# Kernel optimization log

Measured on AMD Instinct MI355X. Metric: run time of the kernel, lower is better.

The kernel has to match this reference:

```python
import jax, jax.numpy as jnp
import numpy as np

K_MODES, L_LAYERS, N_CH, FEAT = 4, 8, 12, 64
BN_EPS = 1e-5


def setup_inputs() -> dict:
    key = jax.random.key(0)
    ks = jax.random.split(key, 12)
    B, T, C, NC = 64, 4096, N_CH, 10
    x = jax.random.normal(ks[0], (B, T, C), jnp.float32)
    # UVMD learnable params (torch init values)
    alpha = jnp.full((L_LAYERS, K_MODES), 100.0, jnp.float32)
    tau = jnp.full((L_LAYERS,), 0.05, jnp.float32)
    omega = jnp.linspace(0.05, 0.45, K_MODES, dtype=jnp.float32)
    def w(k, shape, fan_in):
        return jax.random.normal(k, shape, jnp.float32) * (1.0 / np.sqrt(fan_in))
    # K stacked per-band conv encoders: (K, O, I, kw)
    W1 = w(ks[1], (K_MODES, 32, C, 7), C * 7)
    W2 = w(ks[2], (K_MODES, 64, 32, 5), 32 * 5)
    W3 = w(ks[3], (K_MODES, FEAT, 64, 3), 64 * 3)
    b1 = jnp.zeros((K_MODES, 32)); g1 = jnp.ones((K_MODES, 32)); be1 = jnp.zeros((K_MODES, 32))
    b2 = jnp.zeros((K_MODES, 64)); g2 = jnp.ones((K_MODES, 64)); be2 = jnp.zeros((K_MODES, 64))
    b3 = jnp.zeros((K_MODES, FEAT)); g3 = jnp.ones((K_MODES, FEAT)); be3 = jnp.zeros((K_MODES, FEAT))
    enc_dim = K_MODES * FEAT
    Wc1 = w(ks[4], (128, enc_dim), enc_dim); bc1 = jnp.zeros((128,))
    Wc2 = w(ks[5], (NC, 128), 128); bc2 = jnp.zeros((NC,))
    return dict(x=x, alpha=alpha, tau=tau, omega=omega,
                W1=W1, b1=b1, g1=g1, be1=be1,
                W2=W2, b2=b2, g2=g2, be2=be2,
                W3=W3, b3=b3, g3=g3, be3=be3,
                Wc1=Wc1, bc1=bc1, Wc2=Wc2, bc2=bc2)


def _conv1d(x, w, b):
    # x: (B, Cin, T), w: (O, I, kw), 'same' padding
    pad = (w.shape[-1] - 1) // 2
    y = jax.lax.conv_general_dilated(x, w, (1,), [(pad, pad)],
                                     dimension_numbers=('NCH', 'OIH', 'NCH'))
    return y + b[None, :, None]


def _bn_eval(x, g, b):
    # BatchNorm1d eval with running_mean=0, running_var=1
    return x * (g / jnp.sqrt(1.0 + BN_EPS))[None, :, None] + b[None, :, None]


def _uvmd(x, alpha, tau, omega):
    B, T, C = x.shape
    x_flat = jnp.transpose(x, (0, 2, 1)).reshape(B * C, T)
    X = jnp.fft.rfft(x_flat, n=T)                         # (B*C, T//2+1) complex
    freqs = jnp.linspace(0.0, 0.5, T // 2 + 1).astype(jnp.float32)
    lam = jnp.zeros_like(X)
    u = [jnp.zeros_like(X) for _ in range(K_MODES)]
    total = jnp.zeros_like(X)                             # running sum of u_hats (Gauss-Seidel)
    for l in range(L_LAYERS):
        for k in range(K_MODES):
            residual = X - (total - u[k]) + lam / 2.0
            denom = 1.0 + alpha[l, k] * (freqs - omega[k]) ** 2
            new_u = residual / denom
            total = total - u[k] + new_u
            u[k] = new_u
        lam = lam + tau[l] * (X - total)
    modes = jnp.stack([jnp.fft.irfft(uk, n=T) for uk in u], axis=0)  # (K, B*C, T)
    return modes.reshape(K_MODES, B, C, T).transpose(1, 0, 3, 2)     # (B, K, T, C)


def reference(x, alpha, tau, omega,
              W1, b1, g1, be1, W2, b2, g2, be2, W3, b3, g3, be3,
              Wc1, bc1, Wc2, bc2):
    modes = _uvmd(x, alpha, tau, omega)           # (B, K, T, C)
    xk = jnp.transpose(modes, (1, 0, 3, 2))        # (K, B, C, T)

    def enc_one(xb, w1, bb1, gg1, bbe1, w2, bb2, gg2, bbe2, w3, bb3, gg3, bbe3):
        h = jax.nn.relu(_bn_eval(_conv1d(xb, w1, bb1), gg1, bbe1))
        h = jax.nn.relu(_bn_eval(_conv1d(h, w2, bb2), gg2, bbe2))
        h = jax.nn.relu(_bn_eval(_conv1d(h, w3, bb3), gg3, bbe3))
        return h.mean(axis=-1)                     # AdaptiveAvgPool1d(1)+Flatten -> (B, FEAT)

    feats = jax.vmap(enc_one)(xk, W1, b1, g1, be1, W2, b2, g2, be2, W3, b3, g3, be3)  # (K, B, FEAT)
    features = jnp.transpose(feats, (1, 0, 2)).reshape(feats.shape[1], -1)            # cat over k
    h = jax.nn.relu(features @ Wc1.T + bc1)        # Dropout is identity in eval
    logits = h @ Wc2.T + bc2
    return logits
```

## Files before the change

kernel.cpp:

```cpp
#include <hip/hip_runtime.h>
#include <math.h>

#define T_LEN 4096
#define NBINS 2049
#define B_SZ 64
#define C_IN 12
#define KM 4
#define FEAT 64

typedef __attribute__((ext_vector_type(8))) short short8v;
typedef __attribute__((ext_vector_type(4))) float floatx4;

__device__ __forceinline__ unsigned short f2bf(float f)
{
    unsigned int u = __float_as_uint(f);
    u += 0x7FFFu + ((u >> 16) & 1u);
    return (unsigned short)(u >> 16);
}

__device__ __forceinline__ int fphys(int i) { return i ^ ((i >> 4) & 15); }

__global__ void prep_all(const float* __restrict__ alpha,
                         const float* __restrict__ tau,
                         const float* __restrict__ omega,
                         const float* __restrict__ W1,
                         const float* __restrict__ W2,
                         const float* __restrict__ W3,
                         float2* __restrict__ tw4,
                         float* __restrict__ g,
                         float* __restrict__ feats,
                         unsigned short* __restrict__ Wp1,
                         unsigned short* __restrict__ Wp2,
                         unsigned short* __restrict__ Wp3)
{
    int gid = blockIdx.x * 256 + threadIdx.x;
    if (gid < 4096) {
        float ang = -(float)M_PI * (float)gid / 2048.0f;
        float sn, cs;
        sincosf(ang, &sn, &cs);
        tw4[gid] = make_float2(cs, sn);
        return;
    }
    gid -= 4096;
    if (gid < NBINS) {
        int f = gid;
        float freq = 0.5f * (float)f / 2048.0f;
        float a[4] = {0.f, 0.f, 0.f, 0.f};
        float s = 0.f, lamc = 0.f;
        for (int l = 0; l < 8; ++l) {
            for (int k = 0; k < 4; ++k) {
                float r = 1.f - (s - a[k]) + 0.5f * lamc;
                float d = freq - omega[k];
                float denom = 1.f + alpha[l * 4 + k] * d * d;
                float anew = r / denom;
                s += anew - a[k];
                a[k] = anew;
            }
            lamc += tau[l] * (1.f - s);
        }
        for (int k = 0; k < 4; ++k) g[k * NBINS + f] = a[k];
        return;
    }
    gid -= NBINS;
    if (gid < B_SZ * KM * FEAT) { feats[gid] = 0.f; return; }
    gid -= B_SZ * KM * FEAT;
    if (gid < KM * 4 * 32 * 32) {
        int i = gid;
        int kidx  = i & 31;
        int o     = (i >> 5) & 31;
        int dpair = (i >> 10) & 3;
        int k     = i >> 12;
        int d = dpair * 2 + (kidx >> 4);
        int c = kidx & 15;
        float v = (d < 7 && c < 12) ? W1[(((size_t)k * 32 + o) * 12 + c) * 7 + d] : 0.f;
        Wp1[(size_t)k * 4096 + dpair * 1024 + o * 32 + kidx] = f2bf(v);
        return;
    }
    gid -= KM * 4 * 32 * 32;
    if (gid < KM * 5 * 64 * 32) {
        int i = gid;
        int c = i & 31;
        int o = (i >> 5) & 63;
        int kd = i >> 11;
        int d = kd % 5, k = kd / 5;
        float v = W2[(((size_t)k * 64 + o) * 32 + c) * 5 + d];
        int sr = o >> 1;
        int q = (o & 1) * 4 + (c >> 3);
        int qp = q ^ (sr & 7);
        Wp2[(size_t)(k * 5 + d) * 2048 + sr * 64 + qp * 8 + (c & 7)] = f2bf(v);
        return;
    }
    gid -= KM * 5 * 64 * 32;
    if (gid < KM * 3 * 64 * 64) {
        int i = gid;
        int c = i & 63;
        int o = (i >> 6) & 63;
        int kd = i >> 12;
        int d = kd % 3, k = kd / 3;
        float v = W3[(((size_t)k * 64 + o) * 64 + c) * 3 + d];
        int blk = (c >> 3) ^ (o & 7);
        Wp3[(size_t)k * (3 * 64 * 64) + (d * 64 + o) * 64 + blk * 8 + (c & 7)] = f2bf(v);
        return;
    }
}

__device__ inline float2* fft_stages4(float2* bufA, float2* bufB,
                                      const float2* __restrict__ tw4, float syf)
{
    float2* src = bufA;
    float2* dst = bufB;
#pragma unroll
    for (int st = 0; st < 6; ++st) {
        const int sh = 2 * st;
        const int s = 1 << sh;
        for (int v = threadIdx.x; v < 1024; v += 512) {
            const int q = v & (s - 1);
            const int p = v >> sh;
            float2 a = src[fphys(v)];
            float2 b = src[fphys(v + 1024)];
            float2 c = src[fphys(v + 2048)];
            float2 d = src[fphys(v + 3072)];
            const int i1 = p << sh;
            float2 w1 = tw4[i1];
            float2 w2 = tw4[2 * i1];
            float2 w3 = tw4[3 * i1];
            float apcx = a.x + c.x, apcy = a.y + c.y;
            float amcx = a.x - c.x, amcy = a.y - c.y;
            float bpdx = b.x + d.x, bpdy = b.y + d.y;
            float sjx = -syf * (b.y - d.y);
            float sjy =  syf * (b.x - d.x);
            float2 x0 = make_float2(apcx + bpdx, apcy + bpdy);
            float t1x = amcx - sjx, t1y = amcy - sjy;
            float t2x = apcx - bpdx, t2y = apcy - bpdy;
            float t3x = amcx + sjx, t3y = amcy + sjy;
            float cs1 = w1.x, sn1 = syf * w1.y;
            float cs2 = w2.x, sn2 = syf * w2.y;
            float cs3 = w3.x, sn3 = syf * w3.y;
            float2 x1 = make_float2(cs1 * t1x - sn1 * t1y, cs1 * t1y + sn1 * t1x);
            float2 x2 = make_float2(cs2 * t2x - sn2 * t2y, cs2 * t2y + sn2 * t2x);
            float2 x3 = make_float2(cs3 * t3x - sn3 * t3y, cs3 * t3y + sn3 * t3x);
            const int ob = q + (p << (sh + 2));
            dst[fphys(ob)]         = x0;
            dst[fphys(ob + s)]     = x1;
            dst[fphys(ob + 2 * s)] = x2;
            dst[fphys(ob + 3 * s)] = x3;
        }
        __syncthreads();
        float2* tmp = src; src = dst; dst = tmp;
    }
    return src;
}

__global__ __launch_bounds__(512) void fft_fwd_packed(const float* __restrict__ x,
                                                      const float2* __restrict__ tw4,
                                                      float2* __restrict__ Xs)
{
    int rp = blockIdx.x;
    int b = rp / 6, c0 = (rp % 6) * 2;
    __shared__ float2 bufA[T_LEN];
    __shared__ float2 bufB[T_LEN];
    for (int t = threadIdx.x; t < T_LEN; t += 512) {
        const float* px = x + ((size_t)b * T_LEN + t) * C_IN + c0;
        bufA[fphys(t)] = make_float2(px[0], px[1]);
    }
    __syncthreads();
    float2* Z = fft_stages4(bufA, bufB, tw4, 1.f);
    size_t row = (size_t)b * C_IN + c0;
    for (int f = threadIdx.x; f <= 2048; f += 512) {
        float2 z  = Z[fphys(f)];
        float2 zm = Z[fphys((T_LEN - f) & (T_LEN - 1))];
        Xs[row * NBINS + f]       = make_float2(0.5f * (z.x + zm.x), 0.5f * (z.y - zm.y));
        Xs[(row + 1) * NBINS + f] = make_float2(0.5f * (z.y + zm.y), 0.5f * (zm.x - z.x));
    }
}

__global__ __launch_bounds__(512) void fft_inv_packed(const float2* __restrict__ Xs,
                                                      const float* __restrict__ g,
                                                      const float2* __restrict__ tw4,
                                                      unsigned int* __restrict__ modeU)
{
    int rp = blockIdx.x;
    int kk = blockIdx.y;
    int b = rp / 6, pr = rp % 6;
    int c0 = pr * 2;
    size_t rowa = (size_t)b * C_IN + c0;
    __shared__ float2 bufA[T_LEN];
    __shared__ float2 bufB[T_LEN];
    const float* gk = g + kk * NBINS;
    for (int f = threadIdx.x; f < T_LEN; f += 512) {
        int fe = (f <= 2048) ? f : (T_LEN - f);
        float2 A  = Xs[rowa * NBINS + fe];
        float2 Bv = Xs[(rowa + 1) * NBINS + fe];
        float gv = gk[fe];
        if (f > 2048) { A.y = -A.y; Bv.y = -Bv.y; }
        bufA[fphys(f)] = make_float2(gv * (A.x - Bv.y), gv * (A.y + Bv.x));
    }
    __syncthreads();
    float2* z = fft_stages4(bufA, bufB, tw4, -1.f);
    const float invn = 1.f / (float)T_LEN;
    unsigned int* plane = modeU + (((size_t)kk * B_SZ + b) * 6 + pr) * T_LEN;
    for (int t = threadIdx.x; t < T_LEN; t += 512) {
        float2 zz = z[fphys(t)];
        unsigned int pk = (unsigned int)f2bf(zz.x * invn) |
                          ((unsigned int)f2bf(zz.y * invn) << 16);
        plane[t] = pk;
    }
}

__global__ __launch_bounds__(256) void conv1_mfma(
    const unsigned int* __restrict__ modeU,
    const unsigned short* __restrict__ Wp1all,
    const float* __restrict__ bias,
    const float* __restrict__ gamma,
    const float* __restrict__ beta,
    unsigned short* __restrict__ h1bf)
{
    __shared__ __align__(16) char smem[4352 + 8192];
    char* Xl  = smem;
    char* rep = smem + 4352;

    const int b = blockIdx.y;
    const int kk = blockIdx.z;
    const int t0 = blockIdx.x * 128;
    const int tid = threadIdx.x;
    const unsigned int* planes = modeU + ((size_t)kk * B_SZ + b) * 6 * T_LEN;
    const unsigned short* Wp1 = Wp1all + (size_t)kk * 4096;
    const float* bi = bias + kk * 32;
    const float* ga = gamma + kk * 32;
    const float* be = beta + kk * 32;
    const int sr0 = t0 >> 2;

    for (int i = tid; i < 272; i += 256) {
        int p = i / 34;
        int tc = i % 34;
        int t_base = t0 - 4 + tc * 4;
        unsigned int vv[4] = {0u, 0u, 0u, 0u};
        if (p < 6) {
            const unsigned int* pl = planes + (size_t)p * T_LEN;
            if (t_base >= 0 && t_base + 3 < T_LEN) {
                uint4 v4 = *(const uint4*)(pl + t_base);
                vv[0] = v4.x; vv[1] = v4.y; vv[2] = v4.z; vv[3] = v4.w;
            } else {
#pragma unroll
                for (int e = 0; e < 4; ++e) {
                    int t = t_base + e;
                    vv[e] = (t >= 0 && t < T_LEN) ? pl[t] : 0u;
                }
            }
        }
        int cb = p >> 2, j = p & 3;
        int sr_g = t_base >> 2;
        int ls = sr_g - sr0 + 1;
        int key = sr_g & 7;
#pragma unroll
        for (int e = 0; e < 4; ++e) {
            int q = e * 2 + cb;
            int qp = q ^ key;
            *(unsigned int*)(Xl + (size_t)ls * 128 + qp * 16 + j * 4) = vv[e];
        }
    }

    const int w  = tid >> 6;
    const int l  = tid & 63;
    const int lo = l & 15;
    const int hi = l >> 4;

    short8v Bf[4][2];
#pragma unroll
    for (int dp = 0; dp < 4; ++dp)
#pragma unroll
        for (int n = 0; n < 2; ++n) {
            int o = n * 16 + lo;
            Bf[dp][n] = *(const short8v*)((const char*)Wp1 + dp * 2048 + o * 64 + hi * 16);
        }
    __syncthreads();

    floatx4 acc[2][2];
#pragma unroll
    for (int m = 0; m < 2; ++m)
#pragma unroll
        for (int n = 0; n < 2; ++n)
            acc[m][n] = (floatx4){0.f, 0.f, 0.f, 0.f};

#pragma unroll
    for (int dp = 0; dp < 4; ++dp)
#pragma unroll
        for (int m = 0; m < 2; ++m) {
            int t_in = t0 + w * 32 + m * 16 + lo + dp * 2 + (hi >> 1) - 3;
            int sr_g = t_in >> 2;
            int ls = sr_g - sr0 + 1;
            int q = (t_in & 3) * 2 + (hi & 1);
            int qp = q ^ (sr_g & 7);
            short8v Af = *(const short8v*)(Xl + (size_t)ls * 128 + qp * 16);
#pragma unroll
            for (int n = 0; n < 2; ++n)
                acc[m][n] = __builtin_amdgcn_mfma_f32_16x16x32_bf16(
                    Af, Bf[dp][n], acc[m][n], 0, 0, 0);
        }

    const float rs = 1.f / sqrtf(1.f + 1e-5f);
#pragma unroll
    for (int n = 0; n < 2; ++n) {
        int o = n * 16 + lo;
        float sc = ga[o] * rs;
        float bb = fmaf(bi[o], sc, be[o]);
#pragma unroll
        for (int m = 0; m < 2; ++m)
#pragma unroll
            for (int r = 0; r < 4; ++r) {
                float v = fmaxf(fmaf(acc[m][n][r], sc, bb), 0.f);
                int t_loc = w * 32 + m * 16 + 4 * hi + r;
                int q = (t_loc & 1) * 4 + (o >> 3);
                int qp = q ^ ((t_loc >> 1) & 7);
                *(unsigned short*)(rep + (size_t)(t_loc >> 1) * 128 + qp * 16 +
                                   (o & 7) * 2) = f2bf(v);
            }
    }
    __syncthreads();
    char* dst = (char*)h1bf + ((size_t)kk * B_SZ + b) * (T_LEN * 64) + (size_t)t0 * 64;
    for (int i = tid; i < 512; i += 256)
        ((float4*)dst)[i] = ((float4*)rep)[i];
}

__global__ __launch_bounds__(256) void conv2_mfma(
    const unsigned short* __restrict__ h1bf,
    const unsigned short* __restrict__ Wp2all,
    const float* __restrict__ bias,
    const float* __restrict__ gamma,
    const float* __restrict__ beta,
    unsigned short* __restrict__ h2bf)
{
    __shared__ __align__(16) char smem[9216 + 16384];
    char* Xl  = smem;
    char* rep = smem + 9216;

    const int b = blockIdx.y;
    const int kk = blockIdx.z;
    const int t0 = blockIdx.x * 128;
    const int tid = threadIdx.x;
    const char* src = (const char*)h1bf + ((size_t)kk * B_SZ + b) * (T_LEN * 64);
    const unsigned short* Wp2 = Wp2all + (size_t)kk * 5 * 2048;
    const float* bi = bias + kk * 64;
    const float* ga = gamma + kk * 64;
    const float* be = beta + kk * 64;

    for (int i = tid; i < 576; i += 256) {
        int sr_loc = i >> 3;
        int qp = i & 7;
        int key = (sr_loc + 4) & 7;
        int q = qp ^ key;
        int t = (t0 - 8) + sr_loc * 2 + (q >> 2);
        float4 v = make_float4(0.f, 0.f, 0.f, 0.f);
        if (t >= 0 && t < T_LEN)
            v = *(const float4*)(src + (ptrdiff_t)(t0 - 8) * 64 + (size_t)i * 16);
        *(float4*)(Xl + (size_t)i * 16) = v;
    }

    const int w  = tid >> 6;
    const int l  = tid & 63;
    const int lo = l & 15;
    const int hi = l >> 4;

    short8v Bf[5][4];
#pragma unroll
    for (int d = 0; d < 5; ++d)
#pragma unroll
        for (int n = 0; n < 4; ++n) {
            int o = n * 16 + lo;
            int sr = o >> 1;
            int q = (o & 1) * 4 + hi;
            int qp = q ^ (sr & 7);
            Bf[d][n] = *(const short8v*)((const char*)Wp2 + (size_t)d * 4096 + sr * 128 + qp * 16);
        }
    __syncthreads();

    floatx4 acc[2][4];
#pragma unroll
    for (int m = 0; m < 2; ++m)
#pragma unroll
        for (int n = 0; n < 4; ++n)
            acc[m][n] = (floatx4){0.f, 0.f, 0.f, 0.f};

#pragma unroll
    for (int d = 0; d < 5; ++d)
#pragma unroll
        for (int m = 0; m < 2; ++m) {
            int tl = w * 32 + m * 16 + lo + d + 6;
            int sr = tl >> 1;
            int q = (tl & 1) * 4 + hi;
            int qp = q ^ ((sr + 4) & 7);
            short8v Af = *(const short8v*)(Xl + (size_t)sr * 128 + qp * 16);
#pragma unroll
            for (int n = 0; n < 4; ++n)
                acc[m][n] = __builtin_amdgcn_mfma_f32_16x16x32_bf16(
                    Af, Bf[d][n], acc[m][n], 0, 0, 0);
        }

    const float rs = 1.f / sqrtf(1.f + 1e-5f);
#pragma unroll
    for (int n = 0; n < 4; ++n) {
        int o = n * 16 + lo;
        float sc = ga[o] * rs;
        float bb = fmaf(bi[o], sc, be[o]);
        int cq = o >> 3;
#pragma unroll
        for (int m = 0; m < 2; ++m)
#pragma unroll
            for (int r = 0; r < 4; ++r) {
                float v = fmaxf(fmaf(acc[m][n][r], sc, bb), 0.f);
                int trow = w * 32 + m * 16 + 4 * hi + r;
                *(unsigned short*)(rep + (size_t)trow * 128 +
                                   ((cq ^ (trow & 7)) * 16) + (o & 7) * 2) = f2bf(v);
            }
    }
    __syncthreads();
    char* dst = (char*)h2bf + ((size_t)kk * B_SZ + b) * (T_LEN * 128) + (size_t)t0 * 128;
    for (int i = tid; i < 1024; i += 256)
        *(float4*)(dst + (size_t)i * 16) = *(float4*)(rep + (size_t)i * 16);
}

__global__ __launch_bounds__(256) void conv3_mfma(
    const unsigned short* __restrict__ h2bf,
    const unsigned short* __restrict__ Wp3all,
    const float* __restrict__ bias,
    const float* __restrict__ gamma,
    const float* __restrict__ beta,
    float* __restrict__ feats)
{
    __shared__ __align__(16) char smem[16640];
    char* Xl = smem;

    const int b = blockIdx.y;
    const int kk = blockIdx.z;
    const int t0 = blockIdx.x * 128;
    const int tid = threadIdx.x;
    const unsigned short* Wp = Wp3all + (size_t)kk * 3 * 64 * 64;
    const float* bi = bias + kk * 64;
    const float* ga = gamma + kk * 64;
    const float* be = beta + kk * 64;
    const char* hsrc = (const char*)h2bf + ((size_t)kk * B_SZ + b) * (T_LEN * 128);

    for (int i = tid; i < 1040; i += 256) {
        int row = i >> 3;
        int tg = t0 - 1 + row;
        float4 v = make_float4(0.f, 0.f, 0.f, 0.f);
        if (tg >= 0 && tg < T_LEN)
            v = *(const float4*)(hsrc + (size_t)tg * 128 + (i & 7) * 16);
        *(float4*)(Xl + (size_t)i * 16) = v;
    }

    const int w  = tid >> 6;
    const int l  = tid & 63;
    const int lo = l & 15;
    const int hi = l >> 4;

    short8v Bf[6][4];
#pragma unroll
    for (int d = 0; d < 3; ++d)
#pragma unroll
        for (int ch = 0; ch < 2; ++ch)
#pragma unroll
            for (int n = 0; n < 4; ++n) {
                int o = n * 16 + lo;
                int blk = (4 * ch + hi) ^ (o & 7);
                Bf[d * 2 + ch][n] =
                    *(const short8v*)((const char*)Wp + (size_t)(d * 64 + o) * 128 + blk * 16);
            }
    __syncthreads();

    floatx4 acc[2][4];
#pragma unroll
    for (int m = 0; m < 2; ++m)
#pragma unroll
        for (int n = 0; n < 4; ++n)
            acc[m][n] = (floatx4){0.f, 0.f, 0.f, 0.f};

#pragma unroll
    for (int d = 0; d < 3; ++d)
#pragma unroll
        for (int ch = 0; ch < 2; ++ch) {
#pragma unroll
            for (int m = 0; m < 2; ++m) {
                int tl = w * 32 + m * 16 + lo + d;
                int blk = (4 * ch + hi) ^ ((tl - 1) & 7);
                short8v Af = *(const short8v*)(Xl + (size_t)tl * 128 + blk * 16);
#pragma unroll
                for (int n = 0; n < 4; ++n)
                    acc[m][n] = __builtin_amdgcn_mfma_f32_16x16x32_bf16(
                        Af, Bf[d * 2 + ch][n], acc[m][n], 0, 0, 0);
            }
        }

    const float rs = 1.f / sqrtf(1.f + 1e-5f);
#pragma unroll
    for (int n = 0; n < 4; ++n) {
        int o = n * 16 + lo;
        float sc = ga[o] * rs;
        float bb = fmaf(bi[o], sc, be[o]);
        float s = 0.f;
#pragma unroll
        for (int m = 0; m < 2; ++m)
#pragma unroll
            for (int r = 0; r < 4; ++r)
                s += fmaxf(fmaf(acc[m][n][r], sc, bb), 0.f);
        s += __shfl_xor(s, 16, 64);
        s += __shfl_xor(s, 32, 64);
        if (hi == 0)
            atomicAdd(&feats[b * (KM * FEAT) + kk * FEAT + o], s * (1.f / (float)T_LEN));
    }
}

__global__ __launch_bounds__(128) void classifier_kernel(const float* __restrict__ feats,
                                                         const float* __restrict__ Wc1,
                                                         const float* __restrict__ bc1,
                                                         const float* __restrict__ Wc2,
                                                         const float* __restrict__ bc2,
                                                         float* __restrict__ out)
{
    int b = blockIdx.x;
    int j = threadIdx.x;
    __shared__ float h[128];
    float acc = bc1[j];
    const float* fb = feats + b * 256;
    for (int i = 0; i < 256; ++i) acc = fmaf(fb[i], Wc1[j * 256 + i], acc);
    h[j] = fmaxf(acc, 0.f);
    __syncthreads();
    if (j < 10) {
        float acc2 = bc2[j];
        for (int i = 0; i < 128; ++i) acc2 = fmaf(h[i], Wc2[j * 128 + i], acc2);
        out[b * 10 + j] = acc2;
    }
}

extern "C" void kernel_launch(void* const* d_in, const int* in_sizes, int n_in,
                              void* d_out, int out_size, void* d_ws, size_t ws_size,
                              hipStream_t stream)
{
    const float* x     = (const float*)d_in[0];
    const float* alpha = (const float*)d_in[1];
    const float* tau   = (const float*)d_in[2];
    const float* omega = (const float*)d_in[3];
    const float* W1    = (const float*)d_in[4];
    const float* b1    = (const float*)d_in[5];
    const float* g1    = (const float*)d_in[6];
    const float* be1   = (const float*)d_in[7];
    const float* W2    = (const float*)d_in[8];
    const float* b2    = (const float*)d_in[9];
    const float* g2    = (const float*)d_in[10];
    const float* be2   = (const float*)d_in[11];
    const float* W3    = (const float*)d_in[12];
    const float* b3    = (const float*)d_in[13];
    const float* g3    = (const float*)d_in[14];
    const float* be3   = (const float*)d_in[15];
    const float* Wc1   = (const float*)d_in[16];
    const float* bc1   = (const float*)d_in[17];
    const float* Wc2   = (const float*)d_in[18];
    const float* bc2   = (const float*)d_in[19];

    const int NROWS = B_SZ * C_IN;
    float* ws = (float*)d_ws;
    float2* tw4  = (float2*)ws;
    float* g     = ws + 8192;
    float2* Xs   = (float2*)(ws + 8192 + 4 * NBINS);
    unsigned int* modeU = (unsigned int*)(ws + 8192 + 4 * NBINS + (size_t)NROWS * NBINS * 2);
    unsigned short* h1bf = (unsigned short*)(modeU + (size_t)KM * B_SZ * 6 * T_LEN);
    unsigned short* h2bf = h1bf + (size_t)KM * B_SZ * T_LEN * 32;
    float* feats = (float*)(h2bf + (size_t)KM * B_SZ * T_LEN * 64);
    unsigned short* Wp1 = (unsigned short*)(feats + B_SZ * KM * FEAT);
    unsigned short* Wp2 = Wp1 + KM * 4096;
    unsigned short* Wp3 = Wp2 + KM * 5 * 2048;

    const int PREP_TOT = 4096 + NBINS + B_SZ * KM * FEAT +
                         KM * 4 * 32 * 32 + KM * 5 * 64 * 32 + KM * 3 * 64 * 64;
    prep_all<<<(PREP_TOT + 255) / 256, 256, 0, stream>>>(
        alpha, tau, omega, W1, W2, W3, tw4, g, feats, Wp1, Wp2, Wp3);

    fft_fwd_packed<<<NROWS / 2, 512, 0, stream>>>(x, tw4, Xs);
    fft_inv_packed<<<dim3(NROWS / 2, KM), 512, 0, stream>>>(Xs, g, tw4, modeU);

    conv1_mfma<<<dim3(T_LEN / 128, B_SZ, KM), 256, 0, stream>>>(
        modeU, Wp1, b1, g1, be1, h1bf);
    conv2_mfma<<<dim3(T_LEN / 128, B_SZ, KM), 256, 0, stream>>>(
        h1bf, Wp2, b2, g2, be2, h2bf);
    conv3_mfma<<<dim3(T_LEN / 128, B_SZ, KM), 256, 0, stream>>>(
        h2bf, Wp3, b3, g3, be3, feats);

    classifier_kernel<<<B_SZ, 128, 0, stream>>>(feats, Wc1, bc1, Wc2, bc2, (float*)d_out);
}
```

Baseline: 224.6 us.

## Fuse three conv layers into one kernel with halo recompute in LDS

New measurement: 186.1 us (median of 4 runs). 17.1% less time.

```diff
diff --git a/kernel.cpp b/kernel.cpp
--- a/kernel.cpp
+++ b/kernel.cpp
@@ -207,33 +207,43 @@
     }
 }
 
-__global__ __launch_bounds__(256) void conv1_mfma(
+__global__ __launch_bounds__(256) void fused_conv(
     const unsigned int* __restrict__ modeU,
     const unsigned short* __restrict__ Wp1all,
-    const float* __restrict__ bias,
-    const float* __restrict__ gamma,
-    const float* __restrict__ beta,
-    unsigned short* __restrict__ h1bf)
-{
-    __shared__ __align__(16) char smem[4352 + 8192];
-    char* Xl  = smem;
-    char* rep = smem + 4352;
-
-    const int b = blockIdx.y;
+    const unsigned short* __restrict__ Wp2all,
+    const unsigned short* __restrict__ Wp3all,
+    const float* __restrict__ b1, const float* __restrict__ g1, const float* __restrict__ be1,
+    const float* __restrict__ b2, const float* __restrict__ g2, const float* __restrict__ be2,
+    const float* __restrict__ b3, const float* __restrict__ g3, const float* __restrict__ be3,
+    float* __restrict__ feats)
+{
+    __shared__ __align__(16) char smem[28672];
+    char* Xl1 = smem;
+    char* h2l = smem;
+    char* h1l = smem + 18432;
+
+    const int b  = blockIdx.y;
     const int kk = blockIdx.z;
     const int t0 = blockIdx.x * 128;
     const int tid = threadIdx.x;
+    const int sr0 = t0 >> 2;
+
     const unsigned int* planes = modeU + ((size_t)kk * B_SZ + b) * 6 * T_LEN;
     const unsigned short* Wp1 = Wp1all + (size_t)kk * 4096;
-    const float* bi = bias + kk * 32;
-    const float* ga = gamma + kk * 32;
-    const float* be = beta + kk * 32;
-    const int sr0 = t0 >> 2;
-
-    for (int i = tid; i < 272; i += 256) {
-        int p = i / 34;
-        int tc = i % 34;
-        int t_base = t0 - 4 + tc * 4;
+    const unsigned short* Wp2 = Wp2all + (size_t)kk * 5 * 2048;
+    const unsigned short* Wp3 = Wp3all + (size_t)kk * 3 * 64 * 64;
+
+    const float rs = 1.f / sqrtf(1.f + 1e-5f);
+    const int w  = tid >> 6;
+    const int l  = tid & 63;
+    const int lo = l & 15;
+    const int hi = l >> 4;
+
+    for (int i = tid; i < 336; i += 256) {
+        int p = i / 42;
+        int ls = i % 42;
+        int sr_g = sr0 - 5 + ls;
+        int t_base = sr_g * 4;
         unsigned int vv[4] = {0u, 0u, 0u, 0u};
         if (p < 6) {
             const unsigned int* pl = planes + (size_t)p * T_LEN;
@@ -249,119 +259,62 @@
             }
         }
         int cb = p >> 2, j = p & 3;
-        int sr_g = t_base >> 2;
-        int ls = sr_g - sr0 + 1;
         int key = sr_g & 7;
 #pragma unroll
         for (int e = 0; e < 4; ++e) {
             int q = e * 2 + cb;
             int qp = q ^ key;
-            *(unsigned int*)(Xl + (size_t)ls * 128 + qp * 16 + j * 4) = vv[e];
-        }
-    }
-
-    const int w  = tid >> 6;
-    const int l  = tid & 63;
-    const int lo = l & 15;
-    const int hi = l >> 4;
-
-    short8v Bf[4][2];
+            *(unsigned int*)(Xl1 + (size_t)ls * 128 + qp * 16 + j * 4) = vv[e];
+        }
+    }
+
+    short8v Bf1[4][2];
 #pragma unroll
     for (int dp = 0; dp < 4; ++dp)
 #pragma unroll
         for (int n = 0; n < 2; ++n) {
             int o = n * 16 + lo;
-            Bf[dp][n] = *(const short8v*)((const char*)Wp1 + dp * 2048 + o * 64 + hi * 16);
-        }
-    __syncthreads();
-
-    floatx4 acc[2][2];
-#pragma unroll
-    for (int m = 0; m < 2; ++m)
-#pragma unroll
-        for (int n = 0; n < 2; ++n)
-            acc[m][n] = (floatx4){0.f, 0.f, 0.f, 0.f};
-
-#pragma unroll
-    for (int dp = 0; dp < 4; ++dp)
-#pragma unroll
-        for (int m = 0; m < 2; ++m) {
-            int t_in = t0 + w * 32 + m * 16 + lo + dp * 2 + (hi >> 1) - 3;
+            Bf1[dp][n] = *(const short8v*)((const char*)Wp1 + dp * 2048 + o * 64 + hi * 16);
+        }
+    __syncthreads();
+
+    for (int mt = w; mt < 10; mt += 4) {
+        int tbase = t0 - 16 + mt * 16;
+        floatx4 a1[2];
+        a1[0] = (floatx4){0.f, 0.f, 0.f, 0.f};
+        a1[1] = (floatx4){0.f, 0.f, 0.f, 0.f};
+#pragma unroll
+        for (int dp = 0; dp < 4; ++dp) {
+            int t_in = tbase + lo + dp * 2 + (hi >> 1) - 3;
             int sr_g = t_in >> 2;
-            int ls = sr_g - sr0 + 1;
+            int ls = sr_g - sr0 + 5;
             int q = (t_in & 3) * 2 + (hi & 1);
             int qp = q ^ (sr_g & 7);
-            short8v Af = *(const short8v*)(Xl + (size_t)ls * 128 + qp * 16);
+            short8v Af = *(const short8v*)(Xl1 + (size_t)ls * 128 + qp * 16);
 #pragma unroll
             for (int n = 0; n < 2; ++n)
-                acc[m][n] = __builtin_amdgcn_mfma_f32_16x16x32_bf16(
-                    Af, Bf[dp][n], acc[m][n], 0, 0, 0);
-        }
-
-    const float rs = 1.f / sqrtf(1.f + 1e-5f);
-#pragma unroll
-    for (int n = 0; n < 2; ++n) {
-        int o = n * 16 + lo;
-        float sc = ga[o] * rs;
-        float bb = fmaf(bi[o], sc, be[o]);
-#pragma unroll
-        for (int m = 0; m < 2; ++m)
+                a1[n] = __builtin_amdgcn_mfma_f32_16x16x32_bf16(Af, Bf1[dp][n], a1[n], 0, 0, 0);
+        }
+#pragma unroll
+        for (int n = 0; n < 2; ++n) {
+            int o = n * 16 + lo;
+            float sc = g1[kk * 32 + o] * rs;
+            float bb = fmaf(b1[kk * 32 + o], sc, be1[kk * 32 + o]);
 #pragma unroll
             for (int r = 0; r < 4; ++r) {
-                float v = fmaxf(fmaf(acc[m][n][r], sc, bb), 0.f);
-                int t_loc = w * 32 + m * 16 + 4 * hi + r;
-                int q = (t_loc & 1) * 4 + (o >> 3);
-                int qp = q ^ ((t_loc >> 1) & 7);
-                *(unsigned short*)(rep + (size_t)(t_loc >> 1) * 128 + qp * 16 +
-                                   (o & 7) * 2) = f2bf(v);
-            }
-    }
-    __syncthreads();
-    char* dst = (char*)h1bf + ((size_t)kk * B_SZ + b) * (T_LEN * 64) + (size_t)t0 * 64;
-    for (int i = tid; i < 512; i += 256)
-        ((float4*)dst)[i] = ((float4*)rep)[i];
-}
-
-__global__ __launch_bounds__(256) void conv2_mfma(
-    const unsigned short* __restrict__ h1bf,
-    const unsigned short* __restrict__ Wp2all,
-    const float* __restrict__ bias,
-    const float* __restrict__ gamma,
-    const float* __restrict__ beta,
-    unsigned short* __restrict__ h2bf)
-{
-    __shared__ __align__(16) char smem[9216 + 16384];
-    char* Xl  = smem;
-    char* rep = smem + 9216;
-
-    const int b = blockIdx.y;
-    const int kk = blockIdx.z;
-    const int t0 = blockIdx.x * 128;
-    const int tid = threadIdx.x;
-    const char* src = (const char*)h1bf + ((size_t)kk * B_SZ + b) * (T_LEN * 64);
-    const unsigned short* Wp2 = Wp2all + (size_t)kk * 5 * 2048;
-    const float* bi = bias + kk * 64;
-    const float* ga = gamma + kk * 64;
-    const float* be = beta + kk * 64;
-
-    for (int i = tid; i < 576; i += 256) {
-        int sr_loc = i >> 3;
-        int qp = i & 7;
-        int key = (sr_loc + 4) & 7;
-        int q = qp ^ key;
-        int t = (t0 - 8) + sr_loc * 2 + (q >> 2);
-        float4 v = make_float4(0.f, 0.f, 0.f, 0.f);
-        if (t >= 0 && t < T_LEN)
-            v = *(const float4*)(src + (ptrdiff_t)(t0 - 8) * 64 + (size_t)i * 16);
-        *(float4*)(Xl + (size_t)i * 16) = v;
-    }
-
-    const int w  = tid >> 6;
-    const int l  = tid & 63;
-    const int lo = l & 15;
-    const int hi = l >> 4;
-
-    short8v Bf[5][4];
+                int tl1 = mt * 16 + 4 * hi + r;
+                int tg = t0 - 16 + tl1;
+                float v = (tg >= 0 && tg < T_LEN)
+                              ? fmaxf(fmaf(a1[n][r], sc, bb), 0.f) : 0.f;
+                int s1 = tl1 >> 1;
+                int q = (tl1 & 1) * 4 + (o >> 3);
+                int qp = q ^ (s1 & 7);
+                *(unsigned short*)(h1l + (size_t)s1 * 128 + qp * 16 + (o & 7) * 2) = f2bf(v);
+            }
+        }
+    }
+
+    short8v Bf2[5][4];
 #pragma unroll
     for (int d = 0; d < 5; ++d)
 #pragma unroll
@@ -370,91 +323,44 @@
             int sr = o >> 1;
             int q = (o & 1) * 4 + hi;
             int qp = q ^ (sr & 7);
-            Bf[d][n] = *(const short8v*)((const char*)Wp2 + (size_t)d * 4096 + sr * 128 + qp * 16);
-        }
-    __syncthreads();
-
-    floatx4 acc[2][4];
-#pragma unroll
-    for (int m = 0; m < 2; ++m)
-#pragma unroll
-        for (int n = 0; n < 4; ++n)
-            acc[m][n] = (floatx4){0.f, 0.f, 0.f, 0.f};
-
-#pragma unroll
-    for (int d = 0; d < 5; ++d)
-#pragma unroll
-        for (int m = 0; m < 2; ++m) {
-            int tl = w * 32 + m * 16 + lo + d + 6;
-            int sr = tl >> 1;
-            int q = (tl & 1) * 4 + hi;
-            int qp = q ^ ((sr + 4) & 7);
-            short8v Af = *(const short8v*)(Xl + (size_t)sr * 128 + qp * 16);
+            Bf2[d][n] = *(const short8v*)((const char*)Wp2 + (size_t)d * 4096 + sr * 128 + qp * 16);
+        }
+    __syncthreads();
+
+    for (int mt2 = w; mt2 < 9; mt2 += 4) {
+        floatx4 a2[4];
+#pragma unroll
+        for (int n = 0; n < 4; ++n) a2[n] = (floatx4){0.f, 0.f, 0.f, 0.f};
+#pragma unroll
+        for (int d = 0; d < 5; ++d) {
+            int tl_f = mt2 * 16 + lo + d + 6;
+            int s = tl_f >> 1;
+            int q = (tl_f & 1) * 4 + hi;
+            int qp = q ^ (s & 7);
+            short8v Af = *(const short8v*)(h1l + (size_t)s * 128 + qp * 16);
 #pragma unroll
             for (int n = 0; n < 4; ++n)
-                acc[m][n] = __builtin_amdgcn_mfma_f32_16x16x32_bf16(
-                    Af, Bf[d][n], acc[m][n], 0, 0, 0);
-        }
-
-    const float rs = 1.f / sqrtf(1.f + 1e-5f);
-#pragma unroll
-    for (int n = 0; n < 4; ++n) {
-        int o = n * 16 + lo;
-        float sc = ga[o] * rs;
-        float bb = fmaf(bi[o], sc, be[o]);
-        int cq = o >> 3;
-#pragma unroll
-        for (int m = 0; m < 2; ++m)
+                a2[n] = __builtin_amdgcn_mfma_f32_16x16x32_bf16(Af, Bf2[d][n], a2[n], 0, 0, 0);
+        }
+#pragma unroll
+        for (int n = 0; n < 4; ++n) {
+            int o = n * 16 + lo;
+            float sc = g2[kk * 64 + o] * rs;
+            float bb = fmaf(b2[kk * 64 + o], sc, be2[kk * 64 + o]);
+            int cq = o >> 3;
 #pragma unroll
             for (int r = 0; r < 4; ++r) {
-                float v = fmaxf(fmaf(acc[m][n][r], sc, bb), 0.f);
-                int trow = w * 32 + m * 16 + 4 * hi + r;
-                *(unsigned short*)(rep + (size_t)trow * 128 +
-                                   ((cq ^ (trow & 7)) * 16) + (o & 7) * 2) = f2bf(v);
-            }
-    }
-    __syncthreads();
-    char* dst = (char*)h2bf + ((size_t)kk * B_SZ + b) * (T_LEN * 128) + (size_t)t0 * 128;
-    for (int i = tid; i < 1024; i += 256)
-        *(float4*)(dst + (size_t)i * 16) = *(float4*)(rep + (size_t)i * 16);
-}
-
-__global__ __launch_bounds__(256) void conv3_mfma(
-    const unsigned short* __restrict__ h2bf,
-    const unsigned short* __restrict__ Wp3all,
-    const float* __restrict__ bias,
-    const float* __restrict__ gamma,
-    const float* __restrict__ beta,
-    float* __restrict__ feats)
-{
-    __shared__ __align__(16) char smem[16640];
-    char* Xl = smem;
-
-    const int b = blockIdx.y;
-    const int kk = blockIdx.z;
-    const int t0 = blockIdx.x * 128;
-    const int tid = threadIdx.x;
-    const unsigned short* Wp = Wp3all + (size_t)kk * 3 * 64 * 64;
-    const float* bi = bias + kk * 64;
-    const float* ga = gamma + kk * 64;
-    const float* be = beta + kk * 64;
-    const char* hsrc = (const char*)h2bf + ((size_t)kk * B_SZ + b) * (T_LEN * 128);
-
-    for (int i = tid; i < 1040; i += 256) {
-        int row = i >> 3;
-        int tg = t0 - 1 + row;
-        float4 v = make_float4(0.f, 0.f, 0.f, 0.f);
-        if (tg >= 0 && tg < T_LEN)
-            v = *(const float4*)(hsrc + (size_t)tg * 128 + (i & 7) * 16);
-        *(float4*)(Xl + (size_t)i * 16) = v;
-    }
-
-    const int w  = tid >> 6;
-    const int l  = tid & 63;
-    const int lo = l & 15;
-    const int hi = l >> 4;
-
-    short8v Bf[6][4];
+                int tl2 = mt2 * 16 + 4 * hi + r;
+                int tg = t0 - 8 + tl2;
+                float v = (tg >= 0 && tg < T_LEN)
+                              ? fmaxf(fmaf(a2[n][r], sc, bb), 0.f) : 0.f;
+                int blk = cq ^ (tl2 & 7);
+                *(unsigned short*)(h2l + (size_t)tl2 * 128 + blk * 16 + (o & 7) * 2) = f2bf(v);
+            }
+        }
+    }
+
+    short8v Bf3[6][4];
 #pragma unroll
     for (int d = 0; d < 3; ++d)
 #pragma unroll
@@ -463,8 +369,8 @@
             for (int n = 0; n < 4; ++n) {
                 int o = n * 16 + lo;
                 int blk = (4 * ch + hi) ^ (o & 7);
-                Bf[d * 2 + ch][n] =
-                    *(const short8v*)((const char*)Wp + (size_t)(d * 64 + o) * 128 + blk * 16);
+                Bf3[d * 2 + ch][n] =
+                    *(const short8v*)((const char*)Wp3 + (size_t)(d * 64 + o) * 128 + blk * 16);
             }
     __syncthreads();
 
@@ -482,21 +388,21 @@
 #pragma unroll
             for (int m = 0; m < 2; ++m) {
                 int tl = w * 32 + m * 16 + lo + d;
+                int row = tl + 7;
                 int blk = (4 * ch + hi) ^ ((tl - 1) & 7);
-                short8v Af = *(const short8v*)(Xl + (size_t)tl * 128 + blk * 16);
+                short8v Af = *(const short8v*)(h2l + (size_t)row * 128 + blk * 16);
 #pragma unroll
                 for (int n = 0; n < 4; ++n)
                     acc[m][n] = __builtin_amdgcn_mfma_f32_16x16x32_bf16(
-                        Af, Bf[d * 2 + ch][n], acc[m][n], 0, 0, 0);
-            }
-        }
-
-    const float rs = 1.f / sqrtf(1.f + 1e-5f);
+                        Af, Bf3[d * 2 + ch][n], acc[m][n], 0, 0, 0);
+            }
+        }
+
 #pragma unroll
     for (int n = 0; n < 4; ++n) {
         int o = n * 16 + lo;
-        float sc = ga[o] * rs;
-        float bb = fmaf(bi[o], sc, be[o]);
+        float sc = g3[kk * 64 + o] * rs;
+        float bb = fmaf(b3[kk * 64 + o], sc, be3[kk * 64 + o]);
         float s = 0.f;
 #pragma unroll
         for (int m = 0; m < 2; ++m)
@@ -563,9 +469,7 @@
     float* g     = ws + 8192;
     float2* Xs   = (float2*)(ws + 8192 + 4 * NBINS);
     unsigned int* modeU = (unsigned int*)(ws + 8192 + 4 * NBINS + (size_t)NROWS * NBINS * 2);
-    unsigned short* h1bf = (unsigned short*)(modeU + (size_t)KM * B_SZ * 6 * T_LEN);
-    unsigned short* h2bf = h1bf + (size_t)KM * B_SZ * T_LEN * 32;
-    float* feats = (float*)(h2bf + (size_t)KM * B_SZ * T_LEN * 64);
+    float* feats = (float*)(modeU + (size_t)KM * B_SZ * 6 * T_LEN);
     unsigned short* Wp1 = (unsigned short*)(feats + B_SZ * KM * FEAT);
     unsigned short* Wp2 = Wp1 + KM * 4096;
     unsigned short* Wp3 = Wp2 + KM * 5 * 2048;
@@ -578,12 +482,9 @@
     fft_fwd_packed<<<NROWS / 2, 512, 0, stream>>>(x, tw4, Xs);
     fft_inv_packed<<<dim3(NROWS / 2, KM), 512, 0, stream>>>(Xs, g, tw4, modeU);
 
-    conv1_mfma<<<dim3(T_LEN / 128, B_SZ, KM), 256, 0, stream>>>(
-        modeU, Wp1, b1, g1, be1, h1bf);
-    conv2_mfma<<<dim3(T_LEN / 128, B_SZ, KM), 256, 0, stream>>>(
-        h1bf, Wp2, b2, g2, be2, h2bf);
-    conv3_mfma<<<dim3(T_LEN / 128, B_SZ, KM), 256, 0, stream>>>(
-        h2bf, Wp3, b3, g3, be3, feats);
+    fused_conv<<<dim3(T_LEN / 128, B_SZ, KM), 256, 0, stream>>>(
+        modeU, Wp1, Wp2, Wp3,
+        b1, g1, be1, b2, g2, be2, b3, g3, be3, feats);
 
     classifier_kernel<<<B_SZ, 128, 0, stream>>>(feats, Wc1, bc1, Wc2, bc2, (float*)d_out);
 }
```
